# Performance work log

Hardware: AMD Instinct MI355X
Metric: run time of the kernel (lower is better)

The kernel has to match this reference:

```python
import jax, jax.numpy as jnp
import numpy as np

EPS = 1e-8  # torch F.cosine_similarity eps


def _mp_cos(p, q, w):
    # multi-perspective cosine: p,q (b,s,h), w (l,h) -> (b,s,l)
    pw = p[:, None, :, :] * w[None, :, None, :]   # (b,l,s,h)
    qw = q[:, None, :, :] * w[None, :, None, :]
    num = jnp.sum(pw * qw, axis=-1)
    den = jnp.maximum(jnp.linalg.norm(pw, axis=-1) * jnp.linalg.norm(qw, axis=-1), EPS)
    return (num / den).transpose(0, 2, 1)          # (b,s,l)


def _full(p, q, w, direction):
    # match every step of p against last (fw) / first (bw) step of q
    q_t = q[:, -1, :] if direction == 'fw' else q[:, 0, :]
    return _mp_cos(p, jnp.broadcast_to(q_t[:, None, :], p.shape), w)


def _maxpool(p, q, w):
    pw = p[:, None, :, :] * w[None, :, None, :]    # (b,l,sp,h)
    qw = q[:, None, :, :] * w[None, :, None, :]    # (b,l,sq,h)
    dot = jnp.einsum('blph,blqh->blpq', pw, qw)
    mag = jnp.linalg.norm(pw, axis=-1)[..., None] * jnp.linalg.norm(qw, axis=-1)[:, :, None, :]
    cos = (dot / mag).transpose(0, 2, 3, 1)        # (b,sp,sq,l)
    return cos.max(axis=2), cos.max(axis=1)        # (b,sp,l), (b,sq,l)


def _attentive(p, q, w, att):
    pn = jnp.linalg.norm(p, axis=2)                # (b,sp)
    qn = jnp.linalg.norm(q, axis=2)                # (b,sq)
    cos = jnp.einsum('bph,bqh->bpq', p, q) / (pn[:, :, None] * qn[:, None, :])
    if att == 'mean':
        # weighted sums without materializing (b,sp,sq,h)
        p_vec = jnp.einsum('bph,bpq->bqh', p, cos) / cos.sum(axis=1)[..., None]  # (b,sq,h)
        q_vec = jnp.einsum('bqh,bpq->bph', q, cos) / cos.sum(axis=2)[..., None]  # (b,sp,h)
    else:  # 'max' -- elementwise max requires the broadcasted tensor
        p_vec = (p[:, :, None, :] * cos[..., None]).max(axis=1)  # (b,sq,h)
        q_vec = (q[:, None, :, :] * cos[..., None]).max(axis=2)  # (b,sp,h)
    return _mp_cos(p, q_vec, w), _mp_cos(q, p_vec, w)


def _forward(p, q, W):
    h = W.shape[-1]
    pf, pb = p[..., :h], p[..., h:]
    qf, qb = q[..., :h], q[..., h:]
    mv_p, mv_q = [], []
    # full matching
    mv_p += [_full(pf, qf, W[0], 'fw'), _full(pb, qb, W[1], 'bw')]
    mv_q += [_full(qf, pf, W[0], 'fw'), _full(qb, pb, W[1], 'bw')]
    # maxpool matching
    pp_f, pq_f = _maxpool(pf, qf, W[2])
    pp_b, pq_b = _maxpool(pb, qb, W[3])
    mv_p += [pp_f, pp_b]
    mv_q += [pq_f, pq_b]
    # attentive (mean) matching
    ap_f, aq_f = _attentive(pf, qf, W[4], 'mean')
    ap_b, aq_b = _attentive(pb, qb, W[5], 'mean')
    mv_p += [ap_f, ap_b]
    mv_q += [aq_f, aq_b]
    # max-attentive matching
    mp_f, mq_f = _attentive(pf, qf, W[6], 'max')
    mp_b, mq_b = _attentive(pb, qb, W[7], 'max')
    mv_p += [mp_f, mp_b]
    mv_q += [mq_f, mq_b]
    # dropout is identity at inference (training=False)
    return jnp.concatenate(mv_p, axis=2), jnp.concatenate(mv_q, axis=2)


def setup_inputs() -> dict:
    key = jax.random.key(0)
    k1, k2, k3 = jax.random.split(key, 3)
    B, S, H, L = 32, 64, 300, 20
    p = jax.random.normal(k1, (B, S, 2 * H), dtype=jnp.float32)
    q = jax.random.normal(k2, (B, S, 2 * H), dtype=jnp.float32)
    W = jax.random.uniform(k3, (8, L, H), dtype=jnp.float32)  # torch.rand init
    return {"p": p, "q": q, "W": W}


def reference(p, q, W):
    return _forward(p, q, W)
```

## Files before the change

### kernel.cpp

```cpp
#include <hip/hip_runtime.h>

#define B_ 32
#define S_ 64
#define H_ 300
#define H2_ 600
#define L_ 20
#define ROW_ 160
#define OUTQ_OFF ((size_t)B_ * S_ * ROW_)
#define NEG_INF -3.402823466e38f

#define NB_MP 1280
#define NB_W 188
#define NB_COS 1024

typedef __attribute__((ext_vector_type(8))) _Float16 half8v;
typedef __attribute__((ext_vector_type(4))) _Float16 half4v;
typedef __attribute__((ext_vector_type(4))) float float4v;
typedef __attribute__((ext_vector_type(2))) float float2v;

struct CosS {
  float xq[S_][65];
  float xp[4][68];
  float qn_l[S_];
  float cp[4][S_];
};

__device__ __forceinline__ void cos_body(char* smem, int bid,
                                         const float* __restrict__ P,
                                         const float* __restrict__ Q,
                                         float* __restrict__ cosM,
                                         float* __restrict__ sumpart,
                                         float* __restrict__ sum_q) {
  CosS& S = *(CosS*)smem;
  int x = bid & 7, j = bid >> 3;
  int bd = x + 8 * (j & 7);
  int pg = bid >> 6;
  int b = bd >> 1, dir = bd & 1;
  int t = threadIdx.x;
  int q = t & 63, pr = t >> 6;
  const float* Pb = P + (size_t)b * S_ * H2_ + dir * H_;
  const float* Qb = Q + (size_t)b * S_ * H2_ + dir * H_;
  float dot = 0.f, np2 = 0.f, nq2 = 0.f;
  for (int c0 = 0; c0 < H_; c0 += 64) {
    __syncthreads();
#pragma unroll
    for (int jj = 0; jj < 4; ++jj) {
      int idx = t + 256 * jj;
      int s = idx >> 4, g = idx & 15;
      int h = c0 + 4 * g;
      float4v v = {0.f, 0.f, 0.f, 0.f};
      if (h < 297) v = *(const float4v*)&Qb[(size_t)s * H2_ + h];
      S.xq[s][4 * g + 0] = v.x; S.xq[s][4 * g + 1] = v.y;
      S.xq[s][4 * g + 2] = v.z; S.xq[s][4 * g + 3] = v.w;
    }
    if (t < 64) {
      int s = t >> 4, g = t & 15;
      int h = c0 + 4 * g;
      float4v v = {0.f, 0.f, 0.f, 0.f};
      if (h < 297) v = *(const float4v*)&Pb[(size_t)(pg * 4 + s) * H2_ + h];
      *(float4v*)&S.xp[s][4 * g] = v;
    }
    __syncthreads();
    for (int hh = 0; hh < 64; hh += 4) {
      float4v av = *(const float4v*)&S.xp[pr][hh];
      float q0 = S.xq[q][hh + 0];
      float q1 = S.xq[q][hh + 1];
      float q2 = S.xq[q][hh + 2];
      float q3 = S.xq[q][hh + 3];
      dot = fmaf(av.x, q0, dot); dot = fmaf(av.y, q1, dot);
      dot = fmaf(av.z, q2, dot); dot = fmaf(av.w, q3, dot);
      np2 = fmaf(av.x, av.x, np2); np2 = fmaf(av.y, av.y, np2);
      np2 = fmaf(av.z, av.z, np2); np2 = fmaf(av.w, av.w, np2);
      if (pr == 0) {
        nq2 = fmaf(q0, q0, nq2); nq2 = fmaf(q1, q1, nq2);
        nq2 = fmaf(q2, q2, nq2); nq2 = fmaf(q3, q3, nq2);
      }
    }
  }
  if (pr == 0) S.qn_l[q] = sqrtf(nq2);
  __syncthreads();
  float pn = sqrtf(np2);
  float c = dot / (pn * S.qn_l[q]);
  int p = pg * 4 + pr;
  cosM[(size_t)bd * S_ * S_ + (size_t)p * S_ + q] = c;
  float rs = c;
#pragma unroll
  for (int m = 1; m < 64; m <<= 1) rs += __shfl_xor(rs, m);
  if (q == 0) sum_q[bd * S_ + p] = rs;
  S.cp[pr][q] = c;
  __syncthreads();
  if (t < S_)
    sumpart[((size_t)bd * 16 + pg) * S_ + t] =
        S.cp[0][t] + S.cp[1][t] + S.cp[2][t] + S.cp[3][t];
}

#define HP 72
struct MaxpoolS {
  _Float16 ph[S_][HP];
  _Float16 qh[S_][HP];
  float w1s[H_];
  float pn2[S_], qn2[S_];
  float colp[4][S_];
};

__device__ __forceinline__ void maxpool_body(char* smem, int bid,
                                             const float* __restrict__ P,
                                             const float* __restrict__ Q,
                                             const float* __restrict__ Wf,
                                             float* __restrict__ out) {
  MaxpoolS& S = *(MaxpoolS*)smem;
  int x = bid & 7, j = bid >> 3;
  int bd = x + 8 * (j & 7);
  int l = j >> 3;
  int b = bd >> 1, dir = bd & 1;
  int t = threadIdx.x;
  int w = t >> 6, lane = t & 63, quad = lane >> 4, col = lane & 15;
  const float* wg = Wf + (size_t)(2 + dir) * L_ * H_ + (size_t)l * H_;
  if (t < 75) {
    float4v v = *(const float4v*)&wg[4 * t];
    float4v a = {fabsf(v.x), fabsf(v.y), fabsf(v.z), fabsf(v.w)};
    *(float4v*)&S.w1s[4 * t] = a;
  }
  const float* Pb = P + (size_t)b * S_ * H2_ + dir * H_;
  const float* Qb = Q + (size_t)b * S_ * H2_ + dir * H_;
  float4v acc[4];
#pragma unroll
  for (int qt = 0; qt < 4; ++qt) acc[qt] = (float4v){0.f, 0.f, 0.f, 0.f};
  float np2a[4] = {0.f, 0.f, 0.f, 0.f};
  float nq2a[4] = {0.f, 0.f, 0.f, 0.f};
  for (int h0 = 0; h0 < H_; h0 += 64) {
    __syncthreads();
#pragma unroll
    for (int jj = 0; jj < 4; ++jj) {
      int idx = t + 256 * jj;
      int s = idx >> 4, c4 = idx & 15;
      int h = h0 + 4 * c4;
      float4v pv = {0.f, 0.f, 0.f, 0.f}, qv = {0.f, 0.f, 0.f, 0.f};
      if (h < 297) {
        float4v wv = *(const float4v*)&S.w1s[h];
        float4v p4 = *(const float4v*)&Pb[(size_t)s * H2_ + h];
        float4v q4 = *(const float4v*)&Qb[(size_t)s * H2_ + h];
        pv = p4 * wv;
        qv = q4 * wv;
      }
      half4v phv = __builtin_convertvector(pv, half4v);
      half4v qhv = __builtin_convertvector(qv, half4v);
      *(half4v*)&S.ph[s][4 * c4] = phv;
      *(half4v*)&S.qh[s][4 * c4] = qhv;
      float4v pf = __builtin_convertvector(phv, float4v);
      float4v qf = __builtin_convertvector(qhv, float4v);
      np2a[jj] += pf.x * pf.x + pf.y * pf.y + pf.z * pf.z + pf.w * pf.w;
      nq2a[jj] += qf.x * qf.x + qf.y * qf.y + qf.z * qf.z + qf.w * qf.w;
    }
    __syncthreads();
#pragma unroll
    for (int ks = 0; ks < 2; ++ks) {
      half8v ah = *(const half8v*)&S.ph[16 * w + col][ks * 32 + quad * 8];
#pragma unroll
      for (int qt = 0; qt < 4; ++qt) {
        half8v bh = *(const half8v*)&S.qh[16 * qt + col][ks * 32 + quad * 8];
        acc[qt] = __builtin_amdgcn_mfma_f32_16x16x32_f16(ah, bh, acc[qt], 0, 0, 0);
      }
    }
  }
#pragma unroll
  for (int jj = 0; jj < 4; ++jj) {
    float a = np2a[jj], bb = nq2a[jj];
#pragma unroll
    for (int m = 1; m < 16; m <<= 1) {
      a += __shfl_xor(a, m);
      bb += __shfl_xor(bb, m);
    }
    if ((t & 15) == 0) {
      int s = (t >> 4) + 16 * jj;
      S.pn2[s] = a;
      S.qn2[s] = bb;
    }
  }
  __syncthreads();
  float pnv[4];
#pragma unroll
  for (int r = 0; r < 4; ++r) pnv[r] = sqrtf(S.pn2[16 * w + quad * 4 + r]);
  float rowm[4] = {NEG_INF, NEG_INF, NEG_INF, NEG_INF};
#pragma unroll
  for (int qt = 0; qt < 4; ++qt) {
    float qnv = sqrtf(S.qn2[16 * qt + col]);
    float cmv = NEG_INF;
#pragma unroll
    for (int r = 0; r < 4; ++r) {
      float c = acc[qt][r] / (pnv[r] * qnv);
      rowm[r] = fmaxf(rowm[r], c);
      cmv = fmaxf(cmv, c);
    }
    cmv = fmaxf(cmv, __shfl_xor(cmv, 16));
    cmv = fmaxf(cmv, __shfl_xor(cmv, 32));
    if (quad == 0) S.colp[w][16 * qt + col] = cmv;
  }
#pragma unroll
  for (int m = 1; m < 16; m <<= 1)
#pragma unroll
    for (int r = 0; r < 4; ++r) rowm[r] = fmaxf(rowm[r], __shfl_xor(rowm[r], m));
  if (col == 0) {
#pragma unroll
    for (int r = 0; r < 4; ++r) {
      int p = 16 * w + quad * 4 + r;
      out[((size_t)b * S_ + p) * ROW_ + (2 + dir) * L_ + l] = rowm[r];
    }
  }
  __syncthreads();
  if (t < S_) {
    float m0 = fmaxf(fmaxf(S.colp[0][t], S.colp[1][t]), fmaxf(S.colp[2][t], S.colp[3][t]));
    out[OUTQ_OFF + ((size_t)b * S_ + t) * ROW_ + (2 + dir) * L_ + l] = m0;
  }
}

__global__ __launch_bounds__(256) void k1(const float* __restrict__ P,
                                          const float* __restrict__ Q,
                                          const float* __restrict__ Wf,
                                          float* __restrict__ w2r,
                                          float* __restrict__ cosM,
                                          float* __restrict__ sumpart,
                                          float* __restrict__ sum_q,
                                          float* __restrict__ out) {
  extern __shared__ char smem[];
  int bid = blockIdx.x;
  if (bid < NB_MP) {
    maxpool_body(smem, bid, P, Q, Wf, out);
  } else if (bid < NB_MP + NB_W) {
    int i = (bid - NB_MP) * 256 + threadIdx.x;
    if (i < 8 * L_ * H_) {
      float v = Wf[i];
      w2r[i] = v * v;
    }
  } else {
    cos_body(smem, bid - (NB_MP + NB_W), P, Q, cosM, sumpart, sum_q);
  }
}

#define SG 4
struct OutsS {
  float u[600];
  float xP[SG][H_], xQ[SG][H_];
  float vmq[SG][H_], vmp[SG][H_], vxq[SG][H_], vxp[SG][H_];
  float sps[SG], sqs[SG];
};

__global__ __launch_bounds__(512) void k2(const float* __restrict__ P,
                                          const float* __restrict__ Q,
                                          const float* __restrict__ w2r,
                                          const float* __restrict__ cosM,
                                          const float* __restrict__ sumpart,
                                          const float* __restrict__ sum_q,
                                          float* __restrict__ out) {
  extern __shared__ char smem[];
  OutsS& S = *(OutsS*)smem;
  int bid = blockIdx.x;
  int x = bid & 7, j = bid >> 3;
  int bd = x + 8 * (j & 7);
  int sg = j >> 3;
  int s0 = sg * SG;
  int b = bd >> 1, dir = bd & 1;
  int t = threadIdx.x;
  float (*cosT)[8] = (float (*)[8])&S.u[0];
  const float* cm = cosM + (size_t)bd * S_ * S_;
  {
    int k = t >> 3, jj = t & 7, si = jj & 3;
    cosT[k][jj] = (jj < 4) ? cm[(size_t)k * S_ + s0 + si]
                           : cm[(size_t)(s0 + si) * S_ + k];
  }
  if (t < SG) {
    float a = 0.f;
    for (int pg = 0; pg < 16; ++pg) a += sumpart[((size_t)bd * 16 + pg) * S_ + s0 + t];
    S.sps[t] = a;
    S.sqs[t] = sum_q[bd * S_ + s0 + t];
  }
  int tgt = dir ? 0 : S_ - 1;
  const float* Pb = P + (size_t)b * S_ * H2_ + dir * H_;
  const float* Qb = Q + (size_t)b * S_ * H2_ + dir * H_;
  if (t < SG * 75) {
    int si = t / 75, c4 = t - si * 75;
    *(float4v*)&S.xP[si][4 * c4] = *(const float4v*)&Pb[(size_t)(s0 + si) * H2_ + 4 * c4];
    *(float4v*)&S.xQ[si][4 * c4] = *(const float4v*)&Qb[(size_t)(s0 + si) * H2_ + 4 * c4];
  }
  __syncthreads();
  if (t < H_) {
    int h = t;
    float2v amp01 = {0.f, 0.f}, amp23 = {0.f, 0.f};
    float2v amq01 = {0.f, 0.f}, amq23 = {0.f, 0.f};
    float2v axp01 = {NEG_INF, NEG_INF}, axp23 = {NEG_INF, NEG_INF};
    float2v axq01 = {NEG_INF, NEG_INF}, axq23 = {NEG_INF, NEG_INF};
#pragma unroll 4
    for (int k = 0; k < S_; ++k) {
      float pv = Pb[(size_t)k * H2_ + h];
      float qv = Qb[(size_t)k * H2_ + h];
      float4v cc = *(const float4v*)&cosT[k][0];
      float4v cr = *(const float4v*)&cosT[k][4];
      float2v cc01 = {cc.x, cc.y}, cc23 = {cc.z, cc.w};
      float2v cr01 = {cr.x, cr.y}, cr23 = {cr.z, cr.w};
      float2v m0 = pv * cc01;
      amp01 += m0; axp01 = __builtin_elementwise_max(axp01, m0);
      float2v m1 = pv * cc23;
      amp23 += m1; axp23 = __builtin_elementwise_max(axp23, m1);
      float2v m2 = qv * cr01;
      amq01 += m2; axq01 = __builtin_elementwise_max(axq01, m2);
      float2v m3 = qv * cr23;
      amq23 += m3; axq23 = __builtin_elementwise_max(axq23, m3);
    }
    S.vmq[0][h] = amq01.x / S.sqs[0];
    S.vmq[1][h] = amq01.y / S.sqs[1];
    S.vmq[2][h] = amq23.x / S.sqs[2];
    S.vmq[3][h] = amq23.y / S.sqs[3];
    S.vmp[0][h] = amp01.x / S.sps[0];
    S.vmp[1][h] = amp01.y / S.sps[1];
    S.vmp[2][h] = amp23.x / S.sps[2];
    S.vmp[3][h] = amp23.y / S.sps[3];
    S.vxq[0][h] = axq01.x; S.vxq[1][h] = axq01.y;
    S.vxq[2][h] = axq23.x; S.vxq[3][h] = axq23.y;
    S.vxp[0][h] = axp01.x; S.vxp[1][h] = axp01.y;
    S.vxp[2][h] = axp23.x; S.vxp[3][h] = axp23.y;
  }
  __syncthreads();
  float* tq = &S.u[0];
  float* tp = &S.u[300];
  if (t < 75) {
    *(float4v*)&tq[4 * t] = *(const float4v*)&Qb[(size_t)tgt * H2_ + 4 * t];
    *(float4v*)&tp[4 * t] = *(const float4v*)&Pb[(size_t)tgt * H2_ + 4 * t];
  }
  __syncthreads();
  const int wb_[6] = {0, 0, 4, 4, 6, 6};
  if (t < 480) {
    int job = t;
    int l = job / 24;
    int g = job - l * 24;
    int pr = g >> 2, si = g & 3;
    const float* xv = (pr & 1) ? S.xQ[si] : S.xP[si];
    const float* y;
    if (pr == 0) y = tq;
    else if (pr == 1) y = tp;
    else if (pr == 2) y = S.vmq[si];
    else if (pr == 3) y = S.vmp[si];
    else if (pr == 4) y = S.vxq[si];
    else y = S.vxp[si];
    int widx = wb_[pr] + dir;
    const float* wp = w2r + (size_t)widx * (L_ * H_) + (size_t)l * H_;
    float4v a1v = {0.f, 0.f, 0.f, 0.f};
    float4v a2v = {0.f, 0.f, 0.f, 0.f};
    float4v a3v = {0.f, 0.f, 0.f, 0.f};
    for (int h4 = 0; h4 < H_; h4 += 4) {
      float4v wv = *(const float4v*)&wp[h4];
      float4v xx = *(const float4v*)&xv[h4];
      float4v yy = *(const float4v*)&y[h4];
      float4v wx = wv * xx;
      float4v wy = wv * yy;
      a1v = wx * yy + a1v;
      a2v = wx * xx + a2v;
      a3v = wy * yy + a3v;
    }
    float a1 = (a1v.x + a1v.y) + (a1v.z + a1v.w);
    float a2 = (a2v.x + a2v.y) + (a2v.z + a2v.w);
    float a3 = (a3v.x + a3v.y) + (a3v.z + a3v.w);
    float den = fmaxf(sqrtf(a2) * sqrtf(a3), 1e-8f);
    float c = a1 / den;
    int s = s0 + si;
    size_t base = ((pr & 1) ? OUTQ_OFF : 0) + ((size_t)b * S_ + s) * ROW_;
    out[base + (size_t)widx * L_ + l] = c;
  }
}

extern "C" void kernel_launch(void* const* d_in, const int* in_sizes, int n_in,
                              void* d_out, int out_size, void* d_ws, size_t ws_size,
                              hipStream_t stream) {
  (void)out_size; (void)ws_size;
  int iw = 2;
  for (int i = 0; i < n_in; ++i) if (in_sizes[i] == 8 * L_ * H_) iw = i;
  int io[2] = {0, 1}, k = 0;
  for (int i = 0; i < n_in && k < 2; ++i) if (i != iw) io[k++] = i;
  const float* P  = (const float*)d_in[io[0]];
  const float* Q  = (const float*)d_in[io[1]];
  const float* Wf = (const float*)d_in[iw];
  float* out = (float*)d_out;

  float* ws = (float*)d_ws;
  float* w2r     = ws;
  float* cosM    = w2r + 48000;
  float* sumpart = cosM + 262144;
  float* sum_q   = sumpart + 65536;

  size_t sh1 = sizeof(CosS) > sizeof(MaxpoolS) ? sizeof(CosS) : sizeof(MaxpoolS);
  k1<<<NB_MP + NB_W + NB_COS, 256, sh1, stream>>>(P, Q, Wf, w2r, cosM, sumpart, sum_q, out);
  k2<<<B_ * 2 * 16, 512, sizeof(OutsS), stream>>>(P, Q, w2r, cosM, sumpart, sum_q, out);
}
```

Measured before the change: 138.0 us.

## Overlap full-matching cosine jobs with attention accumulation in k2

The target-step vectors and the sum loads now go into dedicated shared buffers during the initial load phase, which removes one load phase and one barrier. The full-matching cosine jobs (pr 0/1) are handed to idle threads 320-479 while threads 0-299 run the attention accumulation loop, so that work runs concurrently instead of after it. The remaining 320 jobs run after a single barrier. This adds shared memory and an uneven wave workload.

```diff
diff --git a/kernel.cpp b/kernel.cpp
--- a/kernel.cpp
+++ b/kernel.cpp
@@ -240,10 +240,49 @@
 #define SG 4
 struct OutsS {
   float u[600];
+  float ttq[300], ttp[300];
   float xP[SG][H_], xQ[SG][H_];
   float vmq[SG][H_], vmp[SG][H_], vxq[SG][H_], vxp[SG][H_];
   float sps[SG], sqs[SG];
 };
+
+__device__ __forceinline__ void outs_tail_job(const OutsS& S, int l, int pr,
+                                              int si, int dir, int b, int s0,
+                                              const float* __restrict__ w2r,
+                                              float* __restrict__ out) {
+  const float* xv = (pr & 1) ? S.xQ[si] : S.xP[si];
+  const float* y;
+  if (pr == 0) y = S.ttq;
+  else if (pr == 1) y = S.ttp;
+  else if (pr == 2) y = S.vmq[si];
+  else if (pr == 3) y = S.vmp[si];
+  else if (pr == 4) y = S.vxq[si];
+  else y = S.vxp[si];
+  const int wb_[6] = {0, 0, 4, 4, 6, 6};
+  int widx = wb_[pr] + dir;
+  const float* wp = w2r + (size_t)widx * (L_ * H_) + (size_t)l * H_;
+  float4v a1v = {0.f, 0.f, 0.f, 0.f};
+  float4v a2v = {0.f, 0.f, 0.f, 0.f};
+  float4v a3v = {0.f, 0.f, 0.f, 0.f};
+  for (int h4 = 0; h4 < H_; h4 += 4) {
+    float4v wv = *(const float4v*)&wp[h4];
+    float4v xx = *(const float4v*)&xv[h4];
+    float4v yy = *(const float4v*)&y[h4];
+    float4v wx = wv * xx;
+    float4v wy = wv * yy;
+    a1v = wx * yy + a1v;
+    a2v = wx * xx + a2v;
+    a3v = wy * yy + a3v;
+  }
+  float a1 = (a1v.x + a1v.y) + (a1v.z + a1v.w);
+  float a2 = (a2v.x + a2v.y) + (a2v.z + a2v.w);
+  float a3 = (a3v.x + a3v.y) + (a3v.z + a3v.w);
+  float den = fmaxf(sqrtf(a2) * sqrtf(a3), 1e-8f);
+  float c = a1 / den;
+  int s = s0 + si;
+  size_t base = ((pr & 1) ? OUTQ_OFF : 0) + ((size_t)b * S_ + s) * ROW_;
+  out[base + (size_t)widx * L_ + l] = c;
+}
 
 __global__ __launch_bounds__(512) void k2(const float* __restrict__ P,
                                           const float* __restrict__ Q,
@@ -261,6 +300,9 @@
   int s0 = sg * SG;
   int b = bd >> 1, dir = bd & 1;
   int t = threadIdx.x;
+  int tgt = dir ? 0 : S_ - 1;
+  const float* Pb = P + (size_t)b * S_ * H2_ + dir * H_;
+  const float* Qb = Q + (size_t)b * S_ * H2_ + dir * H_;
   float (*cosT)[8] = (float (*)[8])&S.u[0];
   const float* cm = cosM + (size_t)bd * S_ * S_;
   {
@@ -268,19 +310,23 @@
     cosT[k][jj] = (jj < 4) ? cm[(size_t)k * S_ + s0 + si]
                            : cm[(size_t)(s0 + si) * S_ + k];
   }
-  if (t < SG) {
-    float a = 0.f;
-    for (int pg = 0; pg < 16; ++pg) a += sumpart[((size_t)bd * 16 + pg) * S_ + s0 + t];
-    S.sps[t] = a;
-    S.sqs[t] = sum_q[bd * S_ + s0 + t];
-  }
-  int tgt = dir ? 0 : S_ - 1;
-  const float* Pb = P + (size_t)b * S_ * H2_ + dir * H_;
-  const float* Qb = Q + (size_t)b * S_ * H2_ + dir * H_;
   if (t < SG * 75) {
     int si = t / 75, c4 = t - si * 75;
     *(float4v*)&S.xP[si][4 * c4] = *(const float4v*)&Pb[(size_t)(s0 + si) * H2_ + 4 * c4];
     *(float4v*)&S.xQ[si][4 * c4] = *(const float4v*)&Qb[(size_t)(s0 + si) * H2_ + 4 * c4];
+  } else if (t < 375) {
+    int i = t - 300;
+    *(float4v*)&S.ttq[4 * i] = *(const float4v*)&Qb[(size_t)tgt * H2_ + 4 * i];
+  } else if (t < 450) {
+    int i = t - 375;
+    *(float4v*)&S.ttp[4 * i] = *(const float4v*)&Pb[(size_t)tgt * H2_ + 4 * i];
+  } else if (t < 454) {
+    float a = 0.f;
+    int si = t - 450;
+    for (int pg = 0; pg < 16; ++pg) a += sumpart[((size_t)bd * 16 + pg) * S_ + s0 + si];
+    S.sps[si] = a;
+  } else if (t < 458) {
+    S.sqs[t - 454] = sum_q[bd * S_ + s0 + (t - 454)];
   }
   __syncthreads();
   if (t < H_) {
@@ -318,52 +364,17 @@
     S.vxq[2][h] = axq23.x; S.vxq[3][h] = axq23.y;
     S.vxp[0][h] = axp01.x; S.vxp[1][h] = axp01.y;
     S.vxp[2][h] = axp23.x; S.vxp[3][h] = axp23.y;
-  }
-  __syncthreads();
-  float* tq = &S.u[0];
-  float* tp = &S.u[300];
-  if (t < 75) {
-    *(float4v*)&tq[4 * t] = *(const float4v*)&Qb[(size_t)tgt * H2_ + 4 * t];
-    *(float4v*)&tp[4 * t] = *(const float4v*)&Pb[(size_t)tgt * H2_ + 4 * t];
-  }
-  __syncthreads();
-  const int wb_[6] = {0, 0, 4, 4, 6, 6};
-  if (t < 480) {
-    int job = t;
-    int l = job / 24;
-    int g = job - l * 24;
+  } else if (t >= 320 && t < 480) {
+    int jb = t - 320;
+    int l = jb >> 3, g = jb & 7;
     int pr = g >> 2, si = g & 3;
-    const float* xv = (pr & 1) ? S.xQ[si] : S.xP[si];
-    const float* y;
-    if (pr == 0) y = tq;
-    else if (pr == 1) y = tp;
-    else if (pr == 2) y = S.vmq[si];
-    else if (pr == 3) y = S.vmp[si];
-    else if (pr == 4) y = S.vxq[si];
-    else y = S.vxp[si];
-    int widx = wb_[pr] + dir;
-    const float* wp = w2r + (size_t)widx * (L_ * H_) + (size_t)l * H_;
-    float4v a1v = {0.f, 0.f, 0.f, 0.f};
-    float4v a2v = {0.f, 0.f, 0.f, 0.f};
-    float4v a3v = {0.f, 0.f, 0.f, 0.f};
-    for (int h4 = 0; h4 < H_; h4 += 4) {
-      float4v wv = *(const float4v*)&wp[h4];
-      float4v xx = *(const float4v*)&xv[h4];
-      float4v yy = *(const float4v*)&y[h4];
-      float4v wx = wv * xx;
-      float4v wy = wv * yy;
-      a1v = wx * yy + a1v;
-      a2v = wx * xx + a2v;
-      a3v = wy * yy + a3v;
-    }
-    float a1 = (a1v.x + a1v.y) + (a1v.z + a1v.w);
-    float a2 = (a2v.x + a2v.y) + (a2v.z + a2v.w);
-    float a3 = (a3v.x + a3v.y) + (a3v.z + a3v.w);
-    float den = fmaxf(sqrtf(a2) * sqrtf(a3), 1e-8f);
-    float c = a1 / den;
-    int s = s0 + si;
-    size_t base = ((pr & 1) ? OUTQ_OFF : 0) + ((size_t)b * S_ + s) * ROW_;
-    out[base + (size_t)widx * L_ + l] = c;
+    outs_tail_job(S, l, pr, si, dir, b, s0, w2r, out);
+  }
+  __syncthreads();
+  if (t < 320) {
+    int l = t >> 4, g = t & 15;
+    int pr = 2 + (g >> 2), si = g & 3;
+    outs_tail_job(S, l, pr, si, dir, b, s0, w2r, out);
   }
 }
 
```

New measurement: 137.1 us. Within noise of the previous version (-0.6%).
